# Kernel tuning notes

Hardware: AMD Instinct MI355X
Metric: run time of the kernel (lower is better)

## Reference

```python
import jax, jax.numpy as jnp
import numpy as np

N_NODES = 50000


def mean_aggregate(x, src, dst):
    # gather source features, scatter-sum to destinations, divide by in-degree
    msgs = x[src]                                             # [E, D]
    summed = jax.ops.segment_sum(msgs, dst, num_segments=N_NODES)  # [N, D]
    deg = jax.ops.segment_sum(jnp.ones_like(dst, dtype=x.dtype), dst,
                              num_segments=N_NODES)           # [N]
    return summed / jnp.clip(deg, 1.0)[:, None]


def sage_conv(x, src, dst, Wl, Wr, b):
    # PyG SAGEConv (aggr='mean'): lin_l(agg) + lin_r(x); bias only on lin_l
    agg = mean_aggregate(x, src, dst)
    return agg @ Wl + b + x @ Wr


def setup_inputs() -> dict:
    key = jax.random.key(0)
    ks = jax.random.split(key, 8)
    x = jax.random.normal(ks[0], (N_NODES, 64), dtype=jnp.float32)
    edge_index = jax.random.randint(ks[1], (2, 800000), 0, N_NODES, dtype=jnp.int32)
    W1l = jax.random.normal(ks[2], (64, 128), dtype=jnp.float32) * (1.0 / np.sqrt(64))
    W1r = jax.random.normal(ks[3], (64, 128), dtype=jnp.float32) * (1.0 / np.sqrt(64))
    b1 = jnp.zeros((128,), dtype=jnp.float32)
    W2l = jax.random.normal(ks[4], (128, 40), dtype=jnp.float32) * (1.0 / np.sqrt(128))
    W2r = jax.random.normal(ks[5], (128, 40), dtype=jnp.float32) * (1.0 / np.sqrt(128))
    b2 = jnp.zeros((40,), dtype=jnp.float32)
    return {"x": x, "edge_index": edge_index, "W1l": W1l, "W1r": W1r, "b1": b1,
            "W2l": W2l, "W2r": W2r, "b2": b2}


def reference(x, edge_index, W1l, W1r, b1, W2l, W2r, b2):
    src, dst = edge_index[0], edge_index[1]
    h = sage_conv(x, src, dst, W1l, W1r, b1)
    h = jax.nn.relu(h)
    # dropout p=0.5 is identity in eval mode (self.training=False)
    h = sage_conv(h, src, dst, W2l, W2r, b2)
    return h, jax.nn.log_softmax(h, axis=1)
```

## Files before the change

### kernel.cpp

```cpp
#include <hip/hip_runtime.h>
#include <hip/hip_bf16.h>
#include <math.h>

#define N_NODES 50000
#define N_EDGES 800000
#define D0 64
#define D1 128
#define D2 40

#define NB  256
#define NPB 196

typedef short s16x8 __attribute__((ext_vector_type(8)));
typedef float f32x4 __attribute__((ext_vector_type(4)));

static __device__ __forceinline__ unsigned short f2bf(float v) {
    __hip_bfloat16 hb = __float2bfloat16(v);
    return *(unsigned short*)&hb;
}

__global__ __launch_bounds__(256) void prep_kernel(
        const float* __restrict__ x, const int* __restrict__ dst,
        const float* __restrict__ W1l, const float* __restrict__ W1r,
        const float* __restrict__ W2l, const float* __restrict__ W2r,
        unsigned short* __restrict__ xh, int* __restrict__ hist,
        unsigned short* __restrict__ wpk1, unsigned short* __restrict__ wpk2,
        int E, int nCount, int nCast) {
    int b = blockIdx.x, t = threadIdx.x;
    if (b < nCount) {
        __shared__ int h[NB];
        h[t] = 0;
        __syncthreads();
        int e0 = b * 2048;
        for (int i = t; i < 2048; i += 256) {
            int e = e0 + i;
            if (e < E) atomicAdd(&h[(unsigned)dst[e] / NPB], 1);
        }
        __syncthreads();
        hist[b * NB + t] = h[t];
    } else if (b < nCount + nCast) {
        int i = ((b - nCount) * 256 + t) * 4;
        float4 v = *(const float4*)(x + i);
        unsigned o0 = (unsigned)f2bf(v.x) | ((unsigned)f2bf(v.y) << 16);
        unsigned o1 = (unsigned)f2bf(v.z) | ((unsigned)f2bf(v.w) << 16);
        uint2 pk; pk.x = o0; pk.y = o1;
        *(uint2*)(xh + i) = pk;
    } else if (b < nCount + nCast + 8) {
        int f = (b - nCount - nCast) * 4 + (t >> 6);
        int lane = t & 63;
        int nt = f & 7;
        int col = nt * 16 + (lane & 15);
        int kbase = (f >> 3) * 32 + (lane >> 4) * 8;
        unsigned short* o = wpk1 + ((size_t)f * 64 + lane) * 8;
#pragma unroll
        for (int j = 0; j < 8; ++j) {
            int k = kbase + j;
            float w = (k < 64) ? W1r[k * 128 + col] : W1l[(k - 64) * 128 + col];
            o[j] = f2bf(w);
        }
    } else {
        int f = (b - nCount - nCast - 8) * 4 + (t >> 6);
        if (f < 20) {
            int lane = t & 63;
            int nt = f % 5;
            int col = nt * 16 + (lane & 15);
            int kbase = (f / 5) * 32 + (lane >> 4) * 8;
            unsigned short* o = wpk2 + ((size_t)f * 64 + lane) * 8;
#pragma unroll
            for (int j = 0; j < 8; ++j) {
                int k = kbase + j;
                float w = (col < 40) ? W2l[k * 40 + col] : W2r[k * 40 + (col - 40)];
                o[j] = f2bf(w);
            }
        }
    }
}

__global__ void bucket_scan_kernel(const int* __restrict__ hist, int nCount,
                                   int* __restrict__ bbase, int* __restrict__ bcursor) {
    __shared__ int sd[NB];
    int t = threadIdx.x;
    int v = 0;
#pragma unroll 4
    for (int b = 0; b < nCount; ++b) v += hist[b * NB + t];
    sd[t] = v;
    __syncthreads();
    for (int off = 1; off < NB; off <<= 1) {
        int u = (t >= off) ? sd[t - off] : 0;
        __syncthreads();
        sd[t] += u;
        __syncthreads();
    }
    int ex = sd[t] - v;
    bbase[t] = ex;
    bcursor[t] = ex;
}

__global__ __launch_bounds__(256) void bucket_scatter_kernel(
        const int* __restrict__ src, const int* __restrict__ dst,
        int* __restrict__ bcursor, unsigned* __restrict__ ebuf, int E) {
    __shared__ int h[NB];
    __shared__ int base[NB];
    int t = threadIdx.x;
    int e0 = blockIdx.x * 4096;
    h[t] = 0;
    __syncthreads();
    for (int i = t; i < 4096; i += 256) {
        int e = e0 + i;
        if (e < E) atomicAdd(&h[(unsigned)dst[e] / NPB], 1);
    }
    __syncthreads();
    if (h[t] > 0) base[t] = atomicAdd(&bcursor[t], h[t]);
    h[t] = 0;
    __syncthreads();
    for (int i = t; i < 4096; i += 256) {
        int e = e0 + i;
        if (e < E) {
            unsigned d = (unsigned)dst[e];
            unsigned b = d / NPB;
            unsigned ld = d - b * NPB;
            int k = atomicAdd(&h[b], 1);
            ebuf[base[b] + k] = (ld << 17) | (unsigned)src[e];
        }
    }
}

__global__ __launch_bounds__(256) void bucket_fill_kernel(
        const unsigned* __restrict__ ebuf, const int* __restrict__ bbase,
        int* __restrict__ rowptr, int* __restrict__ csr, int E, int N) {
    __shared__ int cnt[256];
    __shared__ int sd[256];
    int b = blockIdx.x, t = threadIdx.x;
    int s0 = bbase[b];
    int s1 = (b < NB - 1) ? bbase[b + 1] : E;
    int lo = b * NPB;
    cnt[t] = 0;
    __syncthreads();
    for (int i = s0 + t; i < s1; i += 256)
        atomicAdd(&cnt[ebuf[i] >> 17], 1);
    __syncthreads();
    int v = cnt[t];
    sd[t] = v;
    __syncthreads();
    for (int off = 1; off < 256; off <<= 1) {
        int u = (t >= off) ? sd[t - off] : 0;
        __syncthreads();
        sd[t] += u;
        __syncthreads();
    }
    int ex = sd[t] - v;
    int node = lo + t;
    if (t < NPB && node < N) rowptr[node] = s0 + ex;
    cnt[t] = s0 + ex;
    __syncthreads();
    for (int i = s0 + t; i < s1; i += 256) {
        unsigned pk = ebuf[i];
        int p = atomicAdd(&cnt[pk >> 17], 1);
        csr[p] = (int)(pk & 0x1FFFFu);
    }
    if (b == NB - 1 && t == 0) rowptr[N] = E;
}


__global__ void agg1_kernel(const unsigned short* __restrict__ xh, const int* __restrict__ rowptr,
                            const int* __restrict__ csr, unsigned short* __restrict__ aggh, int N) {
    int wid = (blockIdx.x * blockDim.x + threadIdx.x) >> 6;
    int lane = threadIdx.x & 63;
    if (wid >= N) return;
    int beg = rowptr[wid], end = rowptr[wid + 1];
    int deg = end - beg;
    int l = lane & 7, g = lane >> 3;
    float acc[8];
#pragma unroll
    for (int k = 0; k < 8; ++k) acc[k] = 0.f;
    int jmax = (deg + 7) >> 3;
    for (int j = 0; j < jmax; j += 2) {
        int s[2]; float w[2];
#pragma unroll
        for (int u = 0; u < 2; ++u) {
            int slot = (j + u) * 8 + g;
            int e = beg + slot;
            e = (e < end) ? e : (end - 1);
            s[u] = csr[e];
            w[u] = (slot < deg) ? 1.f : 0.f;
        }
#pragma unroll
        for (int u = 0; u < 2; ++u) {
            uint4 v = *(const uint4*)(xh + (size_t)s[u] * D0 + l * 8);
            float f0 = __uint_as_float(v.x << 16), f1 = __uint_as_float(v.x & 0xffff0000u);
            float f2 = __uint_as_float(v.y << 16), f3 = __uint_as_float(v.y & 0xffff0000u);
            float f4 = __uint_as_float(v.z << 16), f5 = __uint_as_float(v.z & 0xffff0000u);
            float f6 = __uint_as_float(v.w << 16), f7 = __uint_as_float(v.w & 0xffff0000u);
            acc[0] = fmaf(w[u], f0, acc[0]); acc[1] = fmaf(w[u], f1, acc[1]);
            acc[2] = fmaf(w[u], f2, acc[2]); acc[3] = fmaf(w[u], f3, acc[3]);
            acc[4] = fmaf(w[u], f4, acc[4]); acc[5] = fmaf(w[u], f5, acc[5]);
            acc[6] = fmaf(w[u], f6, acc[6]); acc[7] = fmaf(w[u], f7, acc[7]);
        }
    }
#pragma unroll
    for (int off = 8; off <= 32; off <<= 1) {
#pragma unroll
        for (int k = 0; k < 8; ++k) acc[k] += __shfl_xor(acc[k], off);
    }
    float inv = 1.f / (float)max(deg, 1);
    if (g == 0) {
        unsigned o0 = (unsigned)f2bf(acc[0] * inv) | ((unsigned)f2bf(acc[1] * inv) << 16);
        unsigned o1 = (unsigned)f2bf(acc[2] * inv) | ((unsigned)f2bf(acc[3] * inv) << 16);
        unsigned o2 = (unsigned)f2bf(acc[4] * inv) | ((unsigned)f2bf(acc[5] * inv) << 16);
        unsigned o3 = (unsigned)f2bf(acc[6] * inv) | ((unsigned)f2bf(acc[7] * inv) << 16);
        uint4 pk; pk.x = o0; pk.y = o1; pk.z = o2; pk.w = o3;
        *(uint4*)(aggh + (size_t)wid * D0 + l * 8) = pk;
    }
}


__global__ void agg2_kernel(const unsigned short* __restrict__ p2h, const float* __restrict__ r2,
                            const int* __restrict__ rowptr, const int* __restrict__ csr,
                            float* __restrict__ out, float* __restrict__ out2, int N) {
    int wid = (blockIdx.x * blockDim.x + threadIdx.x) >> 6;
    int lane = threadIdx.x & 63;
    if (wid >= N) return;
    int beg = rowptr[wid], end = rowptr[wid + 1];
    int deg = end - beg;
    int g = lane / 10;
    int l = lane - g * 10;
    bool gv = g < 6;
    float ax = 0.f, ay = 0.f, az = 0.f, aw = 0.f;
    int jmax = (deg + 5) / 6;
    for (int j = 0; j < jmax; j += 4) {
        int s[4]; float w[4];
#pragma unroll
        for (int u = 0; u < 4; ++u) {
            int slot = (j + u) * 6 + g;
            int e = beg + slot;
            e = (e < end) ? e : (end - 1);
            s[u] = csr[e];
            w[u] = (gv && slot < deg) ? 1.f : 0.f;
        }
#pragma unroll
        for (int u = 0; u < 4; ++u) {
            uint2 v = *(const uint2*)(p2h + (size_t)s[u] * D2 + l * 4);
            float f0 = __uint_as_float(v.x << 16), f1 = __uint_as_float(v.x & 0xffff0000u);
            float f2 = __uint_as_float(v.y << 16), f3 = __uint_as_float(v.y & 0xffff0000u);
            ax = fmaf(w[u], f0, ax); ay = fmaf(w[u], f1, ay);
            az = fmaf(w[u], f2, az); aw = fmaf(w[u], f3, aw);
        }
    }
    {
        float bx = __shfl(ax, lane + 30), by = __shfl(ay, lane + 30),
              bz = __shfl(az, lane + 30), bw = __shfl(aw, lane + 30);
        if (g < 3) { ax += bx; ay += by; az += bz; aw += bw; }
        bx = __shfl(ax, lane + 20); by = __shfl(ay, lane + 20);
        bz = __shfl(az, lane + 20); bw = __shfl(aw, lane + 20);
        if (g == 0) { ax += bx; ay += by; az += bz; aw += bw; }
        bx = __shfl(ax, lane + 10); by = __shfl(ay, lane + 10);
        bz = __shfl(az, lane + 10); bw = __shfl(aw, lane + 10);
        if (g == 0) { ax += bx; ay += by; az += bz; aw += bw; }
    }
    float inv = 1.f / (float)max(deg, 1);
    bool wr = (lane < 10);
    float4 h2;
    if (wr) {
        float4 rr = *(const float4*)(r2 + (size_t)wid * D2 + lane * 4);
        h2.x = rr.x + ax * inv; h2.y = rr.y + ay * inv;
        h2.z = rr.z + az * inv; h2.w = rr.w + aw * inv;
        *(float4*)(out + (size_t)wid * D2 + lane * 4) = h2;
    }
    float m = wr ? fmaxf(fmaxf(h2.x, h2.y), fmaxf(h2.z, h2.w)) : -INFINITY;
#pragma unroll
    for (int off = 1; off < 64; off <<= 1) m = fmaxf(m, __shfl_xor(m, off));
    float s = 0.f;
    if (wr) s = expf(h2.x - m) + expf(h2.y - m) + expf(h2.z - m) + expf(h2.w - m);
#pragma unroll
    for (int off = 1; off < 64; off <<= 1) s += __shfl_xor(s, off);
    if (wr) {
        float lg = m + logf(s);
        float4 o; o.x = h2.x - lg; o.y = h2.y - lg; o.z = h2.z - lg; o.w = h2.w - lg;
        *(float4*)(out2 + (size_t)wid * D2 + lane * 4) = o;
    }
}

__global__ __launch_bounds__(256) void gemm1_mfma(
        const unsigned short* __restrict__ xh, const unsigned short* __restrict__ aggh,
        const unsigned short* __restrict__ Wpk, const float* __restrict__ b1,
        unsigned short* __restrict__ h, int N) {
    __shared__ __align__(16) unsigned short As[128 * 136];
    int t = threadIdx.x;
    int r0 = blockIdx.x * 128;
    for (int i = t; i < 2048; i += 256) {
        int r = i >> 4, c = i & 15;
        int gr = r0 + r; gr = (gr < N) ? gr : (N - 1);
        uint4 v = (c < 8) ? ((const uint4*)(xh + (size_t)gr * 64))[c]
                          : ((const uint4*)(aggh + (size_t)gr * 64))[c - 8];
        *(uint4*)(As + r * 136 + c * 8) = v;
    }
    __syncthreads();
    int w = t >> 6, lane = t & 63;
    int l15 = lane & 15, q = lane >> 4;
    f32x4 zero = {0.f, 0.f, 0.f, 0.f};
    f32x4 acc[2][8];
#pragma unroll
    for (int rt = 0; rt < 2; ++rt)
#pragma unroll
        for (int nt = 0; nt < 8; ++nt) acc[rt][nt] = zero;
    const unsigned short* abase = As + (w * 32 + l15) * 136 + q * 8;
#pragma unroll
    for (int ks = 0; ks < 4; ++ks) {
        s16x8 a0 = *(const s16x8*)(abase + ks * 32);
        s16x8 a1 = *(const s16x8*)(abase + 16 * 136 + ks * 32);
        s16x8 b[8];
#pragma unroll
        for (int nt = 0; nt < 8; ++nt)
            b[nt] = *(const s16x8*)(Wpk + ((size_t)(ks * 8 + nt) * 64 + lane) * 8);
#pragma unroll
        for (int nt = 0; nt < 8; ++nt) {
            acc[0][nt] = __builtin_amdgcn_mfma_f32_16x16x32_bf16(a0, b[nt], acc[0][nt], 0, 0, 0);
            acc[1][nt] = __builtin_amdgcn_mfma_f32_16x16x32_bf16(a1, b[nt], acc[1][nt], 0, 0, 0);
        }
    }
    int rbase = r0 + w * 32 + q * 4;
#pragma unroll
    for (int nt = 0; nt < 8; ++nt) {
        int col = nt * 16 + l15;
        float bias = b1[col];
#pragma unroll
        for (int rt = 0; rt < 2; ++rt) {
#pragma unroll
            for (int reg = 0; reg < 4; ++reg) {
                int row = rbase + rt * 16 + reg;
                if (row < N)
                    h[(size_t)row * 128 + col] = f2bf(fmaxf(acc[rt][nt][reg] + bias, 0.f));
            }
        }
    }
}

__global__ __launch_bounds__(256) void gemm2_mfma(
        const unsigned short* __restrict__ hq, const unsigned short* __restrict__ Wpk,
        const float* __restrict__ b2,
        unsigned short* __restrict__ p2h, float* __restrict__ r2, int N) {
    __shared__ __align__(16) unsigned short As[128 * 136];
    int t = threadIdx.x;
    int r0 = blockIdx.x * 128;
    for (int i = t; i < 2048; i += 256) {
        int r = i >> 4, c = i & 15;
        int gr = r0 + r; gr = (gr < N) ? gr : (N - 1);
        uint4 v = ((const uint4*)(hq + (size_t)gr * 128))[c];
        *(uint4*)(As + r * 136 + c * 8) = v;
    }
    __syncthreads();
    int w = t >> 6, lane = t & 63;
    int l15 = lane & 15, q = lane >> 4;
    f32x4 zero = {0.f, 0.f, 0.f, 0.f};
    f32x4 acc[2][5];
#pragma unroll
    for (int rt = 0; rt < 2; ++rt)
#pragma unroll
        for (int nt = 0; nt < 5; ++nt) acc[rt][nt] = zero;
    const unsigned short* abase = As + (w * 32 + l15) * 136 + q * 8;
#pragma unroll
    for (int ks = 0; ks < 4; ++ks) {
        s16x8 a0 = *(const s16x8*)(abase + ks * 32);
        s16x8 a1 = *(const s16x8*)(abase + 16 * 136 + ks * 32);
        s16x8 b[5];
#pragma unroll
        for (int nt = 0; nt < 5; ++nt)
            b[nt] = *(const s16x8*)(Wpk + ((size_t)(ks * 5 + nt) * 64 + lane) * 8);
#pragma unroll
        for (int nt = 0; nt < 5; ++nt) {
            acc[0][nt] = __builtin_amdgcn_mfma_f32_16x16x32_bf16(a0, b[nt], acc[0][nt], 0, 0, 0);
            acc[1][nt] = __builtin_amdgcn_mfma_f32_16x16x32_bf16(a1, b[nt], acc[1][nt], 0, 0, 0);
        }
    }
    int rbase = r0 + w * 32 + q * 4;
#pragma unroll
    for (int nt = 0; nt < 5; ++nt) {
        int col = nt * 16 + l15;
        bool isp = col < 40;
        int oc = isp ? col : (col - 40);
        float bias = isp ? 0.f : b2[oc];
#pragma unroll
        for (int rt = 0; rt < 2; ++rt) {
#pragma unroll
            for (int reg = 0; reg < 4; ++reg) {
                int row = rbase + rt * 16 + reg;
                if (row < N) {
                    float v = acc[rt][nt][reg] + bias;
                    if (isp) p2h[(size_t)row * 40 + oc] = f2bf(v);
                    else     r2[(size_t)row * 40 + oc] = v;
                }
            }
        }
    }
}


extern "C" void kernel_launch(void* const* d_in, const int* in_sizes, int n_in,
                              void* d_out, int out_size, void* d_ws, size_t ws_size,
                              hipStream_t stream) {
    const float* x   = (const float*)d_in[0];
    const int*   ei  = (const int*)d_in[1];
    const float* W1l = (const float*)d_in[2];
    const float* W1r = (const float*)d_in[3];
    const float* b1  = (const float*)d_in[4];
    const float* W2l = (const float*)d_in[5];
    const float* W2r = (const float*)d_in[6];
    const float* b2  = (const float*)d_in[7];
    float* out = (float*)d_out;

    const int N = N_NODES;
    const int E = in_sizes[1] / 2;
    const int* src = ei;
    const int* dst = ei + E;

    char* p = (char*)d_ws;
    auto alloc = [&](size_t bytes) -> void* {
        void* r = (void*)p;
        p += (bytes + 255) & ~(size_t)255;
        return r;
    };
    const int nCount = (E + 2047) / 2048;
    const int nCast  = (N * D0) / 1024;

    int*      rowptr  = (int*)alloc((size_t)(N + 1) * 4);
    int*      csr     = (int*)alloc((size_t)E * 4);
    unsigned* ebuf    = (unsigned*)alloc((size_t)E * 4);
    int*      hist    = (int*)alloc((size_t)nCount * NB * 4);
    int*      bbase   = (int*)alloc(NB * 4);
    int*      bcursor = (int*)alloc(NB * 4);
    unsigned short* xh    = (unsigned short*)alloc((size_t)N * D0 * 2);
    unsigned short* aggh  = (unsigned short*)alloc((size_t)N * D0 * 2);
    unsigned short* hbuf  = (unsigned short*)alloc((size_t)N * D1 * 2);
    unsigned short* wpk1  = (unsigned short*)alloc((size_t)32 * 64 * 8 * 2);
    unsigned short* wpk2  = (unsigned short*)alloc((size_t)20 * 64 * 8 * 2);
    unsigned short* p2h   = (unsigned short*)alloc((size_t)N * D2 * 2);
    float* r2buf = (float*)alloc((size_t)N * D2 * 4);

    prep_kernel<<<nCount + nCast + 8 + 5, 256, 0, stream>>>(
        x, dst, W1l, W1r, W2l, W2r, xh, hist, wpk1, wpk2, E, nCount, nCast);
    bucket_scan_kernel<<<1, NB, 0, stream>>>(hist, nCount, bbase, bcursor);
    bucket_scatter_kernel<<<(E + 4095) / 4096, 256, 0, stream>>>(src, dst, bcursor, ebuf, E);
    bucket_fill_kernel<<<NB, 256, 0, stream>>>(ebuf, bbase, rowptr, csr, E, N);

    agg1_kernel<<<(N * 64 + 255) / 256, 256, 0, stream>>>(xh, rowptr, csr, aggh, N);
    gemm1_mfma<<<(N + 127) / 128, 256, 0, stream>>>(xh, aggh, wpk1, b1, hbuf, N);

    gemm2_mfma<<<(N + 127) / 128, 256, 0, stream>>>(hbuf, wpk2, b2, p2h, r2buf, N);
    agg2_kernel<<<(N * 64 + 255) / 256, 256, 0, stream>>>(p2h, r2buf, rowptr, csr,
                                                          out, out + (size_t)N * D2, N);
}
```

Baseline: 203.6 us.

## Aggregate directly from destination buckets with shared-memory atomics, dropping CSR build

```diff
diff --git a/kernel.cpp b/kernel.cpp
--- a/kernel.cpp
+++ b/kernel.cpp
@@ -18,6 +18,8 @@
     __hip_bfloat16 hb = __float2bfloat16(v);
     return *(unsigned short*)&hb;
 }
+static __device__ __forceinline__ float bf_lo(unsigned u) { return __uint_as_float(u << 16); }
+static __device__ __forceinline__ float bf_hi(unsigned u) { return __uint_as_float(u & 0xffff0000u); }
 
 __global__ __launch_bounds__(256) void prep_kernel(
         const float* __restrict__ x, const int* __restrict__ dst,
@@ -125,158 +127,135 @@
     }
 }
 
-__global__ __launch_bounds__(256) void bucket_fill_kernel(
+__global__ __launch_bounds__(256) void agg1_bucket_kernel(
         const unsigned* __restrict__ ebuf, const int* __restrict__ bbase,
-        int* __restrict__ rowptr, int* __restrict__ csr, int E, int N) {
-    __shared__ int cnt[256];
-    __shared__ int sd[256];
+        const unsigned short* __restrict__ xh, unsigned short* __restrict__ aggh,
+        int E, int N) {
+    __shared__ float acc[NPB * 68];
+    __shared__ int dcnt[NPB];
     int b = blockIdx.x, t = threadIdx.x;
+    for (int i = t; i < NPB * 68; i += 256) acc[i] = 0.f;
+    for (int i = t; i < NPB; i += 256) dcnt[i] = 0;
+    __syncthreads();
     int s0 = bbase[b];
     int s1 = (b < NB - 1) ? bbase[b + 1] : E;
-    int lo = b * NPB;
-    cnt[t] = 0;
-    __syncthreads();
-    for (int i = s0 + t; i < s1; i += 256)
-        atomicAdd(&cnt[ebuf[i] >> 17], 1);
-    __syncthreads();
-    int v = cnt[t];
-    sd[t] = v;
-    __syncthreads();
-    for (int off = 1; off < 256; off <<= 1) {
-        int u = (t >= off) ? sd[t - off] : 0;
-        __syncthreads();
-        sd[t] += u;
-        __syncthreads();
-    }
-    int ex = sd[t] - v;
-    int node = lo + t;
-    if (t < NPB && node < N) rowptr[node] = s0 + ex;
-    cnt[t] = s0 + ex;
-    __syncthreads();
-    for (int i = s0 + t; i < s1; i += 256) {
-        unsigned pk = ebuf[i];
-        int p = atomicAdd(&cnt[pk >> 17], 1);
-        csr[p] = (int)(pk & 0x1FFFFu);
-    }
-    if (b == NB - 1 && t == 0) rowptr[N] = E;
-}
-
-
-__global__ void agg1_kernel(const unsigned short* __restrict__ xh, const int* __restrict__ rowptr,
-                            const int* __restrict__ csr, unsigned short* __restrict__ aggh, int N) {
-    int wid = (blockIdx.x * blockDim.x + threadIdx.x) >> 6;
-    int lane = threadIdx.x & 63;
-    if (wid >= N) return;
-    int beg = rowptr[wid], end = rowptr[wid + 1];
-    int deg = end - beg;
-    int l = lane & 7, g = lane >> 3;
-    float acc[8];
-#pragma unroll
-    for (int k = 0; k < 8; ++k) acc[k] = 0.f;
-    int jmax = (deg + 7) >> 3;
-    for (int j = 0; j < jmax; j += 2) {
-        int s[2]; float w[2];
-#pragma unroll
-        for (int u = 0; u < 2; ++u) {
-            int slot = (j + u) * 8 + g;
-            int e = beg + slot;
-            e = (e < end) ? e : (end - 1);
-            s[u] = csr[e];
-            w[u] = (slot < deg) ? 1.f : 0.f;
-        }
-#pragma unroll
-        for (int u = 0; u < 2; ++u) {
-            uint4 v = *(const uint4*)(xh + (size_t)s[u] * D0 + l * 8);
-            float f0 = __uint_as_float(v.x << 16), f1 = __uint_as_float(v.x & 0xffff0000u);
-            float f2 = __uint_as_float(v.y << 16), f3 = __uint_as_float(v.y & 0xffff0000u);
-            float f4 = __uint_as_float(v.z << 16), f5 = __uint_as_float(v.z & 0xffff0000u);
-            float f6 = __uint_as_float(v.w << 16), f7 = __uint_as_float(v.w & 0xffff0000u);
-            acc[0] = fmaf(w[u], f0, acc[0]); acc[1] = fmaf(w[u], f1, acc[1]);
-            acc[2] = fmaf(w[u], f2, acc[2]); acc[3] = fmaf(w[u], f3, acc[3]);
-            acc[4] = fmaf(w[u], f4, acc[4]); acc[5] = fmaf(w[u], f5, acc[5]);
-            acc[6] = fmaf(w[u], f6, acc[6]); acc[7] = fmaf(w[u], f7, acc[7]);
-        }
-    }
-#pragma unroll
-    for (int off = 8; off <= 32; off <<= 1) {
-#pragma unroll
-        for (int k = 0; k < 8; ++k) acc[k] += __shfl_xor(acc[k], off);
-    }
-    float inv = 1.f / (float)max(deg, 1);
-    if (g == 0) {
-        unsigned o0 = (unsigned)f2bf(acc[0] * inv) | ((unsigned)f2bf(acc[1] * inv) << 16);
-        unsigned o1 = (unsigned)f2bf(acc[2] * inv) | ((unsigned)f2bf(acc[3] * inv) << 16);
-        unsigned o2 = (unsigned)f2bf(acc[4] * inv) | ((unsigned)f2bf(acc[5] * inv) << 16);
-        unsigned o3 = (unsigned)f2bf(acc[6] * inv) | ((unsigned)f2bf(acc[7] * inv) << 16);
-        uint4 pk; pk.x = o0; pk.y = o1; pk.z = o2; pk.w = o3;
-        *(uint4*)(aggh + (size_t)wid * D0 + l * 8) = pk;
-    }
-}
-
-
-__global__ void agg2_kernel(const unsigned short* __restrict__ p2h, const float* __restrict__ r2,
-                            const int* __restrict__ rowptr, const int* __restrict__ csr,
-                            float* __restrict__ out, float* __restrict__ out2, int N) {
-    int wid = (blockIdx.x * blockDim.x + threadIdx.x) >> 6;
-    int lane = threadIdx.x & 63;
-    if (wid >= N) return;
-    int beg = rowptr[wid], end = rowptr[wid + 1];
-    int deg = end - beg;
-    int g = lane / 10;
-    int l = lane - g * 10;
-    bool gv = g < 6;
-    float ax = 0.f, ay = 0.f, az = 0.f, aw = 0.f;
-    int jmax = (deg + 5) / 6;
-    for (int j = 0; j < jmax; j += 4) {
-        int s[4]; float w[4];
-#pragma unroll
-        for (int u = 0; u < 4; ++u) {
-            int slot = (j + u) * 6 + g;
-            int e = beg + slot;
-            e = (e < end) ? e : (end - 1);
-            s[u] = csr[e];
-            w[u] = (gv && slot < deg) ? 1.f : 0.f;
-        }
-#pragma unroll
-        for (int u = 0; u < 4; ++u) {
-            uint2 v = *(const uint2*)(p2h + (size_t)s[u] * D2 + l * 4);
-            float f0 = __uint_as_float(v.x << 16), f1 = __uint_as_float(v.x & 0xffff0000u);
-            float f2 = __uint_as_float(v.y << 16), f3 = __uint_as_float(v.y & 0xffff0000u);
-            ax = fmaf(w[u], f0, ax); ay = fmaf(w[u], f1, ay);
-            az = fmaf(w[u], f2, az); aw = fmaf(w[u], f3, aw);
-        }
-    }
-    {
-        float bx = __shfl(ax, lane + 30), by = __shfl(ay, lane + 30),
-              bz = __shfl(az, lane + 30), bw = __shfl(aw, lane + 30);
-        if (g < 3) { ax += bx; ay += by; az += bz; aw += bw; }
-        bx = __shfl(ax, lane + 20); by = __shfl(ay, lane + 20);
-        bz = __shfl(az, lane + 20); bw = __shfl(aw, lane + 20);
-        if (g == 0) { ax += bx; ay += by; az += bz; aw += bw; }
-        bx = __shfl(ax, lane + 10); by = __shfl(ay, lane + 10);
-        bz = __shfl(az, lane + 10); bw = __shfl(aw, lane + 10);
-        if (g == 0) { ax += bx; ay += by; az += bz; aw += bw; }
-    }
-    float inv = 1.f / (float)max(deg, 1);
-    bool wr = (lane < 10);
-    float4 h2;
-    if (wr) {
-        float4 rr = *(const float4*)(r2 + (size_t)wid * D2 + lane * 4);
-        h2.x = rr.x + ax * inv; h2.y = rr.y + ay * inv;
-        h2.z = rr.z + az * inv; h2.w = rr.w + aw * inv;
-        *(float4*)(out + (size_t)wid * D2 + lane * 4) = h2;
-    }
-    float m = wr ? fmaxf(fmaxf(h2.x, h2.y), fmaxf(h2.z, h2.w)) : -INFINITY;
-#pragma unroll
-    for (int off = 1; off < 64; off <<= 1) m = fmaxf(m, __shfl_xor(m, off));
-    float s = 0.f;
-    if (wr) s = expf(h2.x - m) + expf(h2.y - m) + expf(h2.z - m) + expf(h2.w - m);
-#pragma unroll
-    for (int off = 1; off < 64; off <<= 1) s += __shfl_xor(s, off);
-    if (wr) {
-        float lg = m + logf(s);
-        float4 o; o.x = h2.x - lg; o.y = h2.y - lg; o.z = h2.z - lg; o.w = h2.w - lg;
-        *(float4*)(out2 + (size_t)wid * D2 + lane * 4) = o;
+    int w = t >> 6, lane = t & 63;
+    int es = lane >> 3, l = lane & 7;
+    for (int base = s0 + w * 16; base < s1; base += 64) {
+        int e0 = base + es, e1 = base + 8 + es;
+        bool v0 = e0 < s1, v1 = e1 < s1;
+        unsigned pk0 = v0 ? ebuf[e0] : 0u;
+        unsigned pk1 = v1 ? ebuf[e1] : 0u;
+        uint4 g0, g1;
+        if (v0) g0 = *(const uint4*)(xh + (size_t)(pk0 & 0x1FFFFu) * D0 + l * 8);
+        if (v1) g1 = *(const uint4*)(xh + (size_t)(pk1 & 0x1FFFFu) * D0 + l * 8);
+        if (v0) {
+            float* ap = &acc[(pk0 >> 17) * 68 + l * 8];
+            atomicAdd(ap + 0, bf_lo(g0.x)); atomicAdd(ap + 1, bf_hi(g0.x));
+            atomicAdd(ap + 2, bf_lo(g0.y)); atomicAdd(ap + 3, bf_hi(g0.y));
+            atomicAdd(ap + 4, bf_lo(g0.z)); atomicAdd(ap + 5, bf_hi(g0.z));
+            atomicAdd(ap + 6, bf_lo(g0.w)); atomicAdd(ap + 7, bf_hi(g0.w));
+            if (l == 0) atomicAdd(&dcnt[pk0 >> 17], 1);
+        }
+        if (v1) {
+            float* ap = &acc[(pk1 >> 17) * 68 + l * 8];
+            atomicAdd(ap + 0, bf_lo(g1.x)); atomicAdd(ap + 1, bf_hi(g1.x));
+            atomicAdd(ap + 2, bf_lo(g1.y)); atomicAdd(ap + 3, bf_hi(g1.y));
+            atomicAdd(ap + 4, bf_lo(g1.z)); atomicAdd(ap + 5, bf_hi(g1.z));
+            atomicAdd(ap + 6, bf_lo(g1.w)); atomicAdd(ap + 7, bf_hi(g1.w));
+            if (l == 0) atomicAdd(&dcnt[pk1 >> 17], 1);
+        }
+    }
+    __syncthreads();
+    for (int i = t; i < NPB * 8; i += 256) {
+        int n = i >> 3, c = i & 7;
+        int gn = b * NPB + n;
+        if (gn < N) {
+            float inv = 1.f / (float)max(dcnt[n], 1);
+            const float* ap = &acc[n * 68 + c * 8];
+            uint4 pk;
+            pk.x = (unsigned)f2bf(ap[0] * inv) | ((unsigned)f2bf(ap[1] * inv) << 16);
+            pk.y = (unsigned)f2bf(ap[2] * inv) | ((unsigned)f2bf(ap[3] * inv) << 16);
+            pk.z = (unsigned)f2bf(ap[4] * inv) | ((unsigned)f2bf(ap[5] * inv) << 16);
+            pk.w = (unsigned)f2bf(ap[6] * inv) | ((unsigned)f2bf(ap[7] * inv) << 16);
+            *(uint4*)(aggh + (size_t)gn * D0 + c * 8) = pk;
+        }
+    }
+}
+
+__global__ __launch_bounds__(256) void agg2_bucket_kernel(
+        const unsigned* __restrict__ ebuf, const int* __restrict__ bbase,
+        const unsigned short* __restrict__ p2h, const float* __restrict__ r2,
+        float* __restrict__ out, float* __restrict__ out2, int E, int N) {
+    __shared__ float acc[NPB * 44];
+    __shared__ int dcnt[NPB];
+    int b = blockIdx.x, t = threadIdx.x;
+    for (int i = t; i < NPB * 44; i += 256) acc[i] = 0.f;
+    for (int i = t; i < NPB; i += 256) dcnt[i] = 0;
+    __syncthreads();
+    int s0 = bbase[b];
+    int s1 = (b < NB - 1) ? bbase[b + 1] : E;
+    int w = t >> 6, lane = t & 63;
+    int es = lane / 5, l5 = lane - es * 5;
+    bool lv = es < 12;
+    for (int base = s0 + w * 24; base < s1; base += 96) {
+        int e0 = base + es, e1 = base + 12 + es;
+        bool v0 = lv && (e0 < s1), v1 = lv && (e1 < s1);
+        unsigned pk0 = v0 ? ebuf[e0] : 0u;
+        unsigned pk1 = v1 ? ebuf[e1] : 0u;
+        uint4 g0, g1;
+        if (v0) g0 = *(const uint4*)(p2h + (size_t)(pk0 & 0x1FFFFu) * D2 + l5 * 8);
+        if (v1) g1 = *(const uint4*)(p2h + (size_t)(pk1 & 0x1FFFFu) * D2 + l5 * 8);
+        if (v0) {
+            float* ap = &acc[(pk0 >> 17) * 44 + l5 * 8];
+            atomicAdd(ap + 0, bf_lo(g0.x)); atomicAdd(ap + 1, bf_hi(g0.x));
+            atomicAdd(ap + 2, bf_lo(g0.y)); atomicAdd(ap + 3, bf_hi(g0.y));
+            atomicAdd(ap + 4, bf_lo(g0.z)); atomicAdd(ap + 5, bf_hi(g0.z));
+            atomicAdd(ap + 6, bf_lo(g0.w)); atomicAdd(ap + 7, bf_hi(g0.w));
+            if (l5 == 0) atomicAdd(&dcnt[pk0 >> 17], 1);
+        }
+        if (v1) {
+            float* ap = &acc[(pk1 >> 17) * 44 + l5 * 8];
+            atomicAdd(ap + 0, bf_lo(g1.x)); atomicAdd(ap + 1, bf_hi(g1.x));
+            atomicAdd(ap + 2, bf_lo(g1.y)); atomicAdd(ap + 3, bf_hi(g1.y));
+            atomicAdd(ap + 4, bf_lo(g1.z)); atomicAdd(ap + 5, bf_hi(g1.z));
+            atomicAdd(ap + 6, bf_lo(g1.w)); atomicAdd(ap + 7, bf_hi(g1.w));
+            if (l5 == 0) atomicAdd(&dcnt[pk1 >> 17], 1);
+        }
+    }
+    __syncthreads();
+    int g = lane / 10, l10 = lane - g * 10;
+    for (int n0 = w * 6; n0 < NPB; n0 += 24) {
+        int n = n0 + g;
+        int gn = b * NPB + n;
+        bool act = (g < 6) && (n < NPB) && (gn < N);
+        float4 h2 = {0.f, 0.f, 0.f, 0.f};
+        if (act) {
+            float inv = 1.f / (float)max(dcnt[n], 1);
+            float4 rr = *(const float4*)(r2 + (size_t)gn * D2 + l10 * 4);
+            const float* ap = &acc[n * 44 + l10 * 4];
+            h2.x = rr.x + ap[0] * inv; h2.y = rr.y + ap[1] * inv;
+            h2.z = rr.z + ap[2] * inv; h2.w = rr.w + ap[3] * inv;
+            *(float4*)(out + (size_t)gn * D2 + l10 * 4) = h2;
+        }
+        float m = act ? fmaxf(fmaxf(h2.x, h2.y), fmaxf(h2.z, h2.w)) : -INFINITY;
+        float tmp;
+        tmp = __shfl(m, lane + 5); if (l10 < 5) m = fmaxf(m, tmp);
+        tmp = __shfl(m, lane + 2); if (l10 < 2) m = fmaxf(m, tmp);
+        tmp = __shfl(m, lane + 1); if (l10 == 0) m = fmaxf(m, tmp);
+        tmp = __shfl(m, lane + 4); if (l10 == 0) m = fmaxf(m, tmp);
+        m = __shfl(m, g * 10);
+        float s = act ? (expf(h2.x - m) + expf(h2.y - m) + expf(h2.z - m) + expf(h2.w - m)) : 0.f;
+        tmp = __shfl(s, lane + 5); if (l10 < 5) s += tmp;
+        tmp = __shfl(s, lane + 2); if (l10 < 2) s += tmp;
+        tmp = __shfl(s, lane + 1); if (l10 == 0) s += tmp;
+        tmp = __shfl(s, lane + 4); if (l10 == 0) s += tmp;
+        s = __shfl(s, g * 10);
+        if (act) {
+            float lg = m + logf(s);
+            float4 o; o.x = h2.x - lg; o.y = h2.y - lg; o.z = h2.z - lg; o.w = h2.w - lg;
+            *(float4*)(out2 + (size_t)gn * D2 + l10 * 4) = o;
+        }
     }
 }
 
@@ -422,8 +401,6 @@
     const int nCount = (E + 2047) / 2048;
     const int nCast  = (N * D0) / 1024;
 
-    int*      rowptr  = (int*)alloc((size_t)(N + 1) * 4);
-    int*      csr     = (int*)alloc((size_t)E * 4);
     unsigned* ebuf    = (unsigned*)alloc((size_t)E * 4);
     int*      hist    = (int*)alloc((size_t)nCount * NB * 4);
     int*      bbase   = (int*)alloc(NB * 4);
@@ -440,12 +417,11 @@
         x, dst, W1l, W1r, W2l, W2r, xh, hist, wpk1, wpk2, E, nCount, nCast);
     bucket_scan_kernel<<<1, NB, 0, stream>>>(hist, nCount, bbase, bcursor);
     bucket_scatter_kernel<<<(E + 4095) / 4096, 256, 0, stream>>>(src, dst, bcursor, ebuf, E);
-    bucket_fill_kernel<<<NB, 256, 0, stream>>>(ebuf, bbase, rowptr, csr, E, N);
-
-    agg1_kernel<<<(N * 64 + 255) / 256, 256, 0, stream>>>(xh, rowptr, csr, aggh, N);
+
+    agg1_bucket_kernel<<<NB, 256, 0, stream>>>(ebuf, bbase, xh, aggh, E, N);
     gemm1_mfma<<<(N + 127) / 128, 256, 0, stream>>>(xh, aggh, wpk1, b1, hbuf, N);
 
     gemm2_mfma<<<(N + 127) / 128, 256, 0, stream>>>(hbuf, wpk2, b2, p2h, r2buf, N);
-    agg2_kernel<<<(N * 64 + 255) / 256, 256, 0, stream>>>(p2h, r2buf, rowptr, csr,
-                                                          out, out + (size_t)N * D2, N);
-}
+    agg2_bucket_kernel<<<NB, 256, 0, stream>>>(ebuf, bbase, p2h, r2buf,
+                                               out, out + (size_t)N * D2, E, N);
+}
```

Result: slower. 597.5 us (+193.5%).
